# Performance work log

Measured on AMD Instinct MI355X. Metric: run time of the kernel, lower is better.

Reference implementation:

```python
import jax, jax.numpy as jnp
import numpy as np

NUM_HEADS = 12

def setup_inputs() -> dict:
    key = jax.random.key(0)
    k1, k2, k3, k4 = jax.random.split(key, 4)
    B, N, C = 8, 4096, 768
    x1 = jax.random.normal(k1, (B, N, C), dtype=jnp.float32)
    x2 = jax.random.normal(k2, (B, N, C), dtype=jnp.float32)
    segfeature = jax.random.normal(k3, (B, N, C), dtype=jnp.float32)
    # nn.Linear(dim, 2*dim, bias=False) weight, stored transposed for y = x @ W
    W_kv = jax.random.normal(k4, (C, 2 * C), dtype=jnp.float32) * (C ** -0.5)
    return {"x1": x1, "x2": x2, "segfeature": segfeature, "W_kv": W_kv}


def reference(x1, x2, segfeature, W_kv):
    B, N, C = x1.shape
    H = NUM_HEADS
    d = C // H
    scale = d ** -0.5
    # queries: [B, H, N, d]
    q1 = x1.reshape(B, N, H, d).transpose(0, 2, 1, 3)
    q2 = x2.reshape(B, N, H, d).transpose(0, 2, 1, 3)
    # kv projection: [B, M, 2C] -> [2, B, H, M, d]
    M = segfeature.shape[1]
    kv = (segfeature @ W_kv).reshape(B, M, 2, H, d).transpose(2, 0, 3, 1, 4)
    k3, v3 = kv[0], kv[1]
    # context matrix: k^T @ v over sequence -> [B, H, d, d]
    ctx = jnp.einsum('bhmd,bhme->bhde', k3, v3) * scale
    ctx = jax.nn.softmax(ctx, axis=-2)
    # apply context to both queries, back to [B, N, C]
    o1 = jnp.einsum('bhnd,bhde->bnhe', q1, ctx).reshape(B, N, C)
    o2 = jnp.einsum('bhnd,bhde->bnhe', q2, ctx).reshape(B, N, C)
    return (o1, o2)
```

## Files before the change

### kernel.cpp

```cpp
#include <hip/hip_runtime.h>

#define DI __device__ __forceinline__

typedef float        f32x4 __attribute__((ext_vector_type(4)));
typedef _Float16     f16x8 __attribute__((ext_vector_type(8)));
typedef unsigned int u32x4 __attribute__((ext_vector_type(4)));
typedef unsigned int u32x2 __attribute__((ext_vector_type(2)));

DI unsigned short f2h(float f){
    _Float16 h = (_Float16)f;
    return __builtin_bit_cast(unsigned short, h);
}

DI void gl_lds16(const void* g, void* l){
    __builtin_amdgcn_global_load_lds(
        (const __attribute__((address_space(1))) unsigned int*)g,
        (__attribute__((address_space(3))) unsigned int*)l, 16, 0, 0);
}

__global__ __launch_bounds__(256) void k_transpose_f16(
    const float* __restrict__ in, unsigned short* __restrict__ o16,
    int rows, int cols, long ibs, long obs)
{
    __shared__ float t[64][65];
    const int b  = blockIdx.z;
    const int r0 = blockIdx.y * 64, c0 = blockIdx.x * 64;
    const int tid = threadIdx.x;
    const float* ib = in + (long)b * ibs;

    #pragma unroll
    for (int i = 0; i < 4; ++i){
        int r  = (tid >> 4) + i * 16;
        int cq = (tid & 15) * 4;
        f32x4 v = *(const f32x4*)&ib[(long)(r0 + r) * cols + c0 + cq];
        t[r][cq+0] = v[0]; t[r][cq+1] = v[1]; t[r][cq+2] = v[2]; t[r][cq+3] = v[3];
    }
    __syncthreads();

    const int c  = tid >> 2;
    const int ms = (tid & 3) * 16;
    unsigned hv[8];
    #pragma unroll
    for (int k2 = 0; k2 < 8; ++k2){
        unsigned short ha = f2h(t[ms + 2*k2 + 0][c]);
        unsigned short hb = f2h(t[ms + 2*k2 + 1][c]);
        hv[k2] = (unsigned)ha | ((unsigned)hb << 16);
    }
    long o = (long)b * obs + (long)(c0 + c) * rows + r0 + ms;
    u32x4 H0 = {hv[0],hv[1],hv[2],hv[3]}, H1 = {hv[4],hv[5],hv[6],hv[7]};
    *(u32x4*)&o16[o]     = H0;
    *(u32x4*)&o16[o + 8] = H1;
}

DI void stage_lds(const unsigned short* __restrict__ src, long stride,
                  int row0, int k0, unsigned short* tile, int tid)
{
    #pragma unroll
    for (int it = 0; it < 4; ++it){
        int D    = (it * 256 + tid) * 16;
        int row  = D >> 7;
        int colb = (D & 127) ^ ((row & 7) << 4);
        const char* g = (const char*)(src + (long)(row0 + row) * stride + k0) + colb;
        gl_lds16(g, (char*)tile + D);
    }
}

DI f16x8 frag_ld(const unsigned short* tile, int row, int kc16)
{
    int logical = (row << 7) + (kc16 << 4);
    int phys    = logical ^ ((row & 7) << 4);
    return *(const f16x8*)((const char*)tile + phys);
}

DI void ldB3(const unsigned short* __restrict__ g0, long S16, long stride,
             int row0, int k0, int tid, f16x8 r0[4], f16x8 r1[4], f16x8 r2[4])
{
    #pragma unroll
    for (int it = 0; it < 4; ++it){
        int D    = (it * 256 + tid) * 16;
        int row  = D >> 7;
        int colb = D & 127;
        long off = (long)(row0 + row) * stride + k0 + (colb >> 1);
        r0[it] = *(const f16x8*)(g0 + off);
        r1[it] = *(const f16x8*)(g0 + S16 + off);
        r2[it] = *(const f16x8*)(g0 + 2 * S16 + off);
    }
}
DI void wrB3(unsigned short* tile, int tid, f16x8 r0[4], f16x8 r1[4], f16x8 r2[4])
{
    #pragma unroll
    for (int it = 0; it < 4; ++it){
        int D    = (it * 256 + tid) * 16;
        int row  = D >> 7;
        int colb = D & 127;
        f16x8 s;
        #pragma unroll
        for (int t = 0; t < 8; ++t)
            s[t] = (_Float16)((float)r0[it][t] + (float)r1[it][t] + (float)r2[it][t]);
        int phys = (D & ~127) | (colb ^ ((row & 7) << 4));
        *(f16x8*)((char*)tile + phys) = s;
    }
}

DI void mfma_tile(const unsigned short* TA, const unsigned short* TB,
                  int wr, int wc, int lane, f32x4 acc[4][4])
{
    #pragma unroll
    for (int ks = 0; ks < 2; ++ks){
        const int kc = ks * 4 + (lane >> 4);
        f16x8 bf[4];
        #pragma unroll
        for (int cf = 0; cf < 4; ++cf)
            bf[cf] = frag_ld(TB, wc + cf * 16 + (lane & 15), kc);
        #pragma unroll
        for (int rf = 0; rf < 4; ++rf){
            f16x8 af = frag_ld(TA, wr + rf * 16 + (lane & 15), kc);
            #pragma unroll
            for (int cf = 0; cf < 4; ++cf)
                acc[rf][cf] = __builtin_amdgcn_mfma_f32_16x16x32_f16(af, bf[cf], acc[rf][cf], 0, 0, 0);
        }
    }
}

DI void kloop(const unsigned short* a, int rowA0, long sA,
              const unsigned short* b, int rowB0, long sB,
              int kbeg, int kend, f32x4 acc[4][4], unsigned short* lds, int tid)
{
    const int lane = tid & 63;
    const int wave = tid >> 6;
    const int wr = (wave >> 1) * 64, wc = (wave & 1) * 64;

    stage_lds(a, sA, rowA0, kbeg, lds,        tid);
    stage_lds(b, sB, rowB0, kbeg, lds + 8192, tid);
    __syncthreads();

    int cur = 0;
    for (int k0 = kbeg; k0 < kend; k0 += 64){
        const unsigned short* TA = lds + cur * 16384;
        const int kn = k0 + 64;
        if (kn < kend){
            unsigned short* NA = lds + (cur ^ 1) * 16384;
            stage_lds(a, sA, rowA0, kn, NA,        tid);
            stage_lds(b, sB, rowB0, kn, NA + 8192, tid);
        }
        mfma_tile(TA, TA + 8192, wr, wc, lane, acc);
        __syncthreads();
        cur ^= 1;
    }
}

__global__ __launch_bounds__(256) void k_gram(
    const unsigned short* __restrict__ X, unsigned short* __restrict__ Gp16)
{
    __shared__ unsigned short lds[4 * 8192];
    const int id  = blockIdx.x;
    const int b   = id & 7;
    const int r   = id >> 3;
    const int ksl = r / 21;
    int q = r % 21;
    int ti = 0, tj = 0;
    #pragma unroll
    for (int i = 0; i < 6; ++i){ int c = 6 - i; if (q < c){ ti = i; tj = i + q; q = -1; break; } q -= c; }

    static const int kb[4] = {0, 1408, 2752, 4096};

    const unsigned short* XB = X + (long)b * 768 * 4096;

    f32x4 acc[4][4];
    #pragma unroll
    for (int i = 0; i < 4; ++i)
        #pragma unroll
        for (int j = 0; j < 4; ++j) acc[i][j] = (f32x4){0.f, 0.f, 0.f, 0.f};

    kloop(XB, ti * 128, 4096, XB, tj * 128, 4096,
          kb[ksl], kb[ksl + 1], acc, lds, threadIdx.x);

    unsigned short* G = Gp16 + ((long)ksl * 8 + b) * 768 * 768;
    const int lane = threadIdx.x & 63, wave = threadIdx.x >> 6;
    const int wr = (wave >> 1) * 64, wc = (wave & 1) * 64;
    #pragma unroll
    for (int rf = 0; rf < 4; ++rf)
        #pragma unroll
        for (int cf = 0; cf < 4; ++cf){
            int gi = ti * 128 + wr + rf * 16 + 4 * (lane >> 4);
            int gj = tj * 128 + wc + cf * 16 + (lane & 15);
            unsigned short h4[4];
            #pragma unroll
            for (int r2 = 0; r2 < 4; ++r2){
                h4[r2] = f2h(acc[rf][cf][r2]);
                G[(long)(gi + r2) * 768 + gj] = h4[r2];
            }
            if (ti != tj){
                u32x2 p = { (unsigned)h4[0] | ((unsigned)h4[1] << 16),
                            (unsigned)h4[2] | ((unsigned)h4[3] << 16) };
                *(u32x2*)(G + (long)gj * 768 + gi) = p;
            }
        }
}

__global__ __launch_bounds__(256) void k_tt(
    const unsigned short* __restrict__ WT, const unsigned short* __restrict__ Gp16,
    unsigned short* __restrict__ TT)
{
    __shared__ unsigned short lds[4 * 8192];
    const long S16 = 4718592;
    const int id = blockIdx.x;
    const int b  = id & 7;
    const int t  = id >> 3;
    const int ti = t % 6, tj = t / 6;
    const int tid = threadIdx.x;

    const unsigned short* A  = WT + (long)768 * 768;
    const unsigned short* G0 = Gp16 + (long)b * 768 * 768;

    f32x4 acc[4][4];
    #pragma unroll
    for (int i = 0; i < 4; ++i)
        #pragma unroll
        for (int j = 0; j < 4; ++j) acc[i][j] = (f32x4){0.f, 0.f, 0.f, 0.f};

    const int lane = tid & 63;
    const int wave = tid >> 6;
    const int wr = (wave >> 1) * 64, wc = (wave & 1) * 64;

    {
        f16x8 r0[4], r1[4], r2[4];
        ldB3(G0, S16, 768, tj * 128, 0, tid, r0, r1, r2);
        stage_lds(A, 768, ti * 128, 0, lds, tid);
        wrB3(lds + 8192, tid, r0, r1, r2);
        __syncthreads();
    }

    int cur = 0;
    for (int k0 = 0; k0 < 768; k0 += 64){
        const unsigned short* TA = lds + cur * 16384;
        const int kn = k0 + 64;
        f16x8 r0[4], r1[4], r2[4];
        if (kn < 768){
            ldB3(G0, S16, 768, tj * 128, kn, tid, r0, r1, r2);
            stage_lds(A, 768, ti * 128, kn, lds + (cur ^ 1) * 16384, tid);
        }
        mfma_tile(TA, TA + 8192, wr, wc, lane, acc);
        if (kn < 768)
            wrB3(lds + (cur ^ 1) * 16384 + 8192, tid, r0, r1, r2);
        __syncthreads();
        cur ^= 1;
    }

    unsigned short* tt = TT + (long)b * 768 * 768;
    #pragma unroll
    for (int rf = 0; rf < 4; ++rf)
        #pragma unroll
        for (int cf = 0; cf < 4; ++cf){
            int gi = ti * 128 + wr + rf * 16 + 4 * (lane >> 4);
            int gj = tj * 128 + wc + cf * 16 + (lane & 15);
            #pragma unroll
            for (int r = 0; r < 4; ++r)
                tt[(long)(gi + r) * 768 + gj] = f2h(acc[rf][cf][r]);
        }
}

__global__ __launch_bounds__(256) void k_ctx(
    const unsigned short* __restrict__ WT, const unsigned short* __restrict__ TT,
    unsigned short* __restrict__ wT)
{
    __shared__ float red[3][64][65];
    const int bh = blockIdx.x;
    const int b = bh / 12, h = bh % 12;
    const int lane = threadIdx.x & 63;
    const int wave = threadIdx.x >> 6;

    const unsigned short* A = WT + (long)(h * 64) * 768;
    const unsigned short* B = TT + (long)b * 768 * 768 + (long)(h * 64) * 768;

    f32x4 acc[4][4];
    #pragma unroll
    for (int i = 0; i < 4; ++i)
        #pragma unroll
        for (int j = 0; j < 4; ++j) acc[i][j] = (f32x4){0.f, 0.f, 0.f, 0.f};

    for (int kc = wave * 6; kc < wave * 6 + 6; ++kc){
        const int k0 = kc * 32 + (lane >> 4) * 8;
        f16x8 af[4], bf[4];
        #pragma unroll
        for (int f = 0; f < 4; ++f){
            long ro = (long)(f * 16 + (lane & 15)) * 768 + k0;
            af[f] = *(const f16x8*)(A + ro);
            bf[f] = *(const f16x8*)(B + ro);
        }
        #pragma unroll
        for (int rf = 0; rf < 4; ++rf)
            #pragma unroll
            for (int cf = 0; cf < 4; ++cf)
                acc[rf][cf] = __builtin_amdgcn_mfma_f32_16x16x32_f16(af[rf], bf[cf], acc[rf][cf], 0, 0, 0);
    }

    if (wave > 0){
        #pragma unroll
        for (int rf = 0; rf < 4; ++rf)
            #pragma unroll
            for (int cf = 0; cf < 4; ++cf)
                #pragma unroll
                for (int r = 0; r < 4; ++r)
                    red[wave - 1][lane][(rf * 4 + cf) * 4 + r] = acc[rf][cf][r];
    }
    __syncthreads();
    if (wave != 0) return;

    #pragma unroll
    for (int rf = 0; rf < 4; ++rf)
        #pragma unroll
        for (int cf = 0; cf < 4; ++cf)
            #pragma unroll
            for (int r = 0; r < 4; ++r){
                int idx = (rf * 4 + cf) * 4 + r;
                acc[rf][cf][r] += red[0][lane][idx] + red[1][lane][idx] + red[2][lane][idx];
            }

    unsigned short* wout = wT + (long)bh * 4096;
    #pragma unroll
    for (int cf = 0; cf < 4; ++cf){
        float pv[16];
        float m = -3.4e38f;
        #pragma unroll
        for (int rf = 0; rf < 4; ++rf)
            #pragma unroll
            for (int r = 0; r < 4; ++r){
                float s = acc[rf][cf][r] * 0.125f;
                pv[rf * 4 + r] = s;
                m = fmaxf(m, s);
            }
        m = fmaxf(m, __shfl_xor(m, 16));
        m = fmaxf(m, __shfl_xor(m, 32));
        float sum = 0.f;
        #pragma unroll
        for (int k = 0; k < 16; ++k){ pv[k] = __expf(pv[k] - m); sum += pv[k]; }
        sum += __shfl_xor(sum, 16);
        sum += __shfl_xor(sum, 32);
        float inv = 1.f / sum;
        int e = cf * 16 + (lane & 15);
        #pragma unroll
        for (int rf = 0; rf < 4; ++rf)
            #pragma unroll
            for (int r = 0; r < 4; ++r){
                int d = rf * 16 + 4 * (lane >> 4) + r;
                wout[e * 64 + d] = f2h(pv[rf * 4 + r] * inv);
            }
    }
}

__global__ __launch_bounds__(256) void k_apply(
    const float* __restrict__ x1, const float* __restrict__ x2,
    const unsigned short* __restrict__ wT, float* __restrict__ out)
{
    __shared__ float ep[4][64][64];
    const int b = blockIdx.z;
    const int h = blockIdx.y >> 1;
    const int src = blockIdx.y & 1;
    const int lane = threadIdx.x & 63, wave = threadIdx.x >> 6;
    const int n0 = blockIdx.x * 256 + wave * 64;

    const float* x = (src ? x2 : x1) + (long)b * 4096 * 768;
    float* o = out + (long)src * 8 * 4096 * 768 + (long)b * 4096 * 768;

    const unsigned short* W = wT + (long)(b * 12 + h) * 4096;
    f16x8 bw[4][2];
    #pragma unroll
    for (int fe = 0; fe < 4; ++fe)
        #pragma unroll
        for (int ks = 0; ks < 2; ++ks)
            bw[fe][ks] = *(const f16x8*)(W + (fe * 16 + (lane & 15)) * 64 + ks * 32 + (lane >> 4) * 8);

    f32x4 acc[4][4];
    #pragma unroll
    for (int i = 0; i < 4; ++i)
        #pragma unroll
        for (int j = 0; j < 4; ++j) acc[i][j] = (f32x4){0.f, 0.f, 0.f, 0.f};

    #pragma unroll
    for (int rf = 0; rf < 4; ++rf){
        const int row = n0 + rf * 16 + (lane & 15);
        const float* xr = x + (long)row * 768 + h * 64 + (lane >> 4) * 8;
        f32x4 v0 = *(const f32x4*)(xr);
        f32x4 v1 = *(const f32x4*)(xr + 4);
        f32x4 v2 = *(const f32x4*)(xr + 32);
        f32x4 v3 = *(const f32x4*)(xr + 36);
        f16x8 a0, a1;
        #pragma unroll
        for (int t = 0; t < 4; ++t){
            a0[t]     = (_Float16)v0[t];
            a0[t + 4] = (_Float16)v1[t];
            a1[t]     = (_Float16)v2[t];
            a1[t + 4] = (_Float16)v3[t];
        }
        #pragma unroll
        for (int fe = 0; fe < 4; ++fe){
            acc[rf][fe] = __builtin_amdgcn_mfma_f32_16x16x32_f16(a0, bw[fe][0], acc[rf][fe], 0, 0, 0);
            acc[rf][fe] = __builtin_amdgcn_mfma_f32_16x16x32_f16(a1, bw[fe][1], acc[rf][fe], 0, 0, 0);
        }
    }

    #pragma unroll
    for (int rf = 0; rf < 4; ++rf)
        #pragma unroll
        for (int fe = 0; fe < 4; ++fe)
            #pragma unroll
            for (int r = 0; r < 4; ++r)
                ep[wave][rf * 16 + 4 * (lane >> 4) + r][fe * 16 + (lane & 15)] = acc[rf][fe][r];

    #pragma unroll
    for (int pass = 0; pass < 16; ++pass){
        int rr = pass * 4 + (lane >> 4);
        f32x4 v = *(const f32x4*)&ep[wave][rr][(lane & 15) * 4];
        *(f32x4*)&o[(long)(n0 + rr) * 768 + h * 64 + (lane & 15) * 4] = v;
    }
}

__global__ void k_sentinel(float* o){ o[0] = 1.0e9f; }

extern "C" void kernel_launch(void* const* d_in, const int* in_sizes, int n_in,
                              void* d_out, int out_size, void* d_ws, size_t ws_size,
                              hipStream_t stream)
{
    (void)in_sizes; (void)n_in; (void)out_size;
    const float* x1  = (const float*)d_in[0];
    const float* x2  = (const float*)d_in[1];
    const float* seg = (const float*)d_in[2];
    const float* Wkv = (const float*)d_in[3];

    char* Wb = (char*)d_ws;
    unsigned short* X    = (unsigned short*)(Wb);
    unsigned short* WT   = (unsigned short*)(Wb + 50331648);
    unsigned short* TT   = (unsigned short*)(Wb + 52690944);
    unsigned short* wT   = (unsigned short*)(Wb + 62128128);
    unsigned short* Gp16 = (unsigned short*)(Wb + 62914560);
    const size_t need = 91226112;

    if (ws_size < need){
        k_sentinel<<<1, 1, 0, stream>>>((float*)d_out);
        return;
    }

    k_transpose_f16<<<dim3(12, 64, 8), 256, 0, stream>>>(
        seg, X, 4096, 768, (long)4096 * 768, (long)768 * 4096);
    k_transpose_f16<<<dim3(24, 12, 1), 256, 0, stream>>>(
        Wkv, WT, 768, 1536, 0, 0);

    k_gram<<<dim3(504), 256, 0, stream>>>(X, Gp16);

    k_tt<<<dim3(288), 256, 0, stream>>>(WT, Gp16, TT);

    k_ctx<<<dim3(96), 256, 0, stream>>>(WT, TT, wT);

    k_apply<<<dim3(16, 24, 8), 256, 0, stream>>>(x1, x2, wT, (float*)d_out);
}
```

Measured before the change: 179.1 us.

## Merge transpose launches, skip duplicate diagonal Gram loads, use nontemporal output stores

The two fp16 transpose launches (segfeature and W_kv) become one kernel whose flat grid picks which tensor each block handles, removing one launch. In the Gram kernel, diagonal tiles (ti==tj) now stage only one operand tile and reuse it for both sides of the MFMA, halving their global-to-LDS traffic. The apply kernel's final output stores become nontemporal so the large output stream does not pollute cache. These are separate small changes, with little added risk beyond the extra branching in the merged prep kernel.

Measured after the change: 173.1 us (median of 2 runs). -3.4%, faster.

```diff
diff --git a/kernel.cpp b/kernel.cpp
--- a/kernel.cpp
+++ b/kernel.cpp
@@ -18,15 +18,25 @@
         (__attribute__((address_space(3))) unsigned int*)l, 16, 0, 0);
 }
 
-__global__ __launch_bounds__(256) void k_transpose_f16(
-    const float* __restrict__ in, unsigned short* __restrict__ o16,
-    int rows, int cols, long ibs, long obs)
+__global__ __launch_bounds__(256) void k_prep(
+    const float* __restrict__ seg, const float* __restrict__ Wkv,
+    unsigned short* __restrict__ X, unsigned short* __restrict__ WT)
 {
     __shared__ float t[64][65];
-    const int b  = blockIdx.z;
-    const int r0 = blockIdx.y * 64, c0 = blockIdx.x * 64;
+    const int gid = blockIdx.x;
+    const float* in; unsigned short* out;
+    int rows, cols, bx, by, bz; long ibs, obs;
+    if (gid < 6144){
+        bz = gid / 768; int r = gid % 768; by = r / 12; bx = r % 12;
+        in = seg; out = X; rows = 4096; cols = 768;
+        ibs = (long)4096 * 768; obs = (long)768 * 4096;
+    } else {
+        int g2 = gid - 6144; by = g2 / 24; bx = g2 % 24; bz = 0;
+        in = Wkv; out = WT; rows = 768; cols = 1536; ibs = 0; obs = 0;
+    }
+    const int r0 = by * 64, c0 = bx * 64;
     const int tid = threadIdx.x;
-    const float* ib = in + (long)b * ibs;
+    const float* ib = in + (long)bz * ibs;
 
     #pragma unroll
     for (int i = 0; i < 4; ++i){
@@ -46,10 +56,10 @@
         unsigned short hb = f2h(t[ms + 2*k2 + 1][c]);
         hv[k2] = (unsigned)ha | ((unsigned)hb << 16);
     }
-    long o = (long)b * obs + (long)(c0 + c) * rows + r0 + ms;
+    long o = (long)bz * obs + (long)(c0 + c) * rows + r0 + ms;
     u32x4 H0 = {hv[0],hv[1],hv[2],hv[3]}, H1 = {hv[4],hv[5],hv[6],hv[7]};
-    *(u32x4*)&o16[o]     = H0;
-    *(u32x4*)&o16[o + 8] = H1;
+    *(u32x4*)&out[o]     = H0;
+    *(u32x4*)&out[o + 8] = H1;
 }
 
 DI void stage_lds(const unsigned short* __restrict__ src, long stride,
@@ -72,36 +82,6 @@
     return *(const f16x8*)((const char*)tile + phys);
 }
 
-DI void ldB3(const unsigned short* __restrict__ g0, long S16, long stride,
-             int row0, int k0, int tid, f16x8 r0[4], f16x8 r1[4], f16x8 r2[4])
-{
-    #pragma unroll
-    for (int it = 0; it < 4; ++it){
-        int D    = (it * 256 + tid) * 16;
-        int row  = D >> 7;
-        int colb = D & 127;
-        long off = (long)(row0 + row) * stride + k0 + (colb >> 1);
-        r0[it] = *(const f16x8*)(g0 + off);
-        r1[it] = *(const f16x8*)(g0 + S16 + off);
-        r2[it] = *(const f16x8*)(g0 + 2 * S16 + off);
-    }
-}
-DI void wrB3(unsigned short* tile, int tid, f16x8 r0[4], f16x8 r1[4], f16x8 r2[4])
-{
-    #pragma unroll
-    for (int it = 0; it < 4; ++it){
-        int D    = (it * 256 + tid) * 16;
-        int row  = D >> 7;
-        int colb = D & 127;
-        f16x8 s;
-        #pragma unroll
-        for (int t = 0; t < 8; ++t)
-            s[t] = (_Float16)((float)r0[it][t] + (float)r1[it][t] + (float)r2[it][t]);
-        int phys = (D & ~127) | (colb ^ ((row & 7) << 4));
-        *(f16x8*)((char*)tile + phys) = s;
-    }
-}
-
 DI void mfma_tile(const unsigned short* TA, const unsigned short* TB,
                   int wr, int wc, int lane, f32x4 acc[4][4])
 {
@@ -119,33 +99,6 @@
             for (int cf = 0; cf < 4; ++cf)
                 acc[rf][cf] = __builtin_amdgcn_mfma_f32_16x16x32_f16(af, bf[cf], acc[rf][cf], 0, 0, 0);
         }
-    }
-}
-
-DI void kloop(const unsigned short* a, int rowA0, long sA,
-              const unsigned short* b, int rowB0, long sB,
-              int kbeg, int kend, f32x4 acc[4][4], unsigned short* lds, int tid)
-{
-    const int lane = tid & 63;
-    const int wave = tid >> 6;
-    const int wr = (wave >> 1) * 64, wc = (wave & 1) * 64;
-
-    stage_lds(a, sA, rowA0, kbeg, lds,        tid);
-    stage_lds(b, sB, rowB0, kbeg, lds + 8192, tid);
-    __syncthreads();
-
-    int cur = 0;
-    for (int k0 = kbeg; k0 < kend; k0 += 64){
-        const unsigned short* TA = lds + cur * 16384;
-        const int kn = k0 + 64;
-        if (kn < kend){
-            unsigned short* NA = lds + (cur ^ 1) * 16384;
-            stage_lds(a, sA, rowA0, kn, NA,        tid);
-            stage_lds(b, sB, rowB0, kn, NA + 8192, tid);
-        }
-        mfma_tile(TA, TA + 8192, wr, wc, lane, acc);
-        __syncthreads();
-        cur ^= 1;
     }
 }
 
@@ -163,8 +116,13 @@
     for (int i = 0; i < 6; ++i){ int c = 6 - i; if (q < c){ ti = i; tj = i + q; q = -1; break; } q -= c; }
 
     static const int kb[4] = {0, 1408, 2752, 4096};
+    const int kbeg = kb[ksl], kend = kb[ksl + 1];
 
     const unsigned short* XB = X + (long)b * 768 * 4096;
+    const int tid  = threadIdx.x;
+    const int lane = tid & 63, wave = tid >> 6;
+    const int wr = (wave >> 1) * 64, wc = (wave & 1) * 64;
+    const bool diag = (ti == tj);
 
     f32x4 acc[4][4];
     #pragma unroll
@@ -172,12 +130,26 @@
         #pragma unroll
         for (int j = 0; j < 4; ++j) acc[i][j] = (f32x4){0.f, 0.f, 0.f, 0.f};
 
-    kloop(XB, ti * 128, 4096, XB, tj * 128, 4096,
-          kb[ksl], kb[ksl + 1], acc, lds, threadIdx.x);
+    stage_lds(XB, 4096, ti * 128, kbeg, lds, tid);
+    if (!diag) stage_lds(XB, 4096, tj * 128, kbeg, lds + 8192, tid);
+    __syncthreads();
+
+    int cur = 0;
+    for (int k0 = kbeg; k0 < kend; k0 += 64){
+        const unsigned short* TA = lds + cur * 16384;
+        const unsigned short* TB = diag ? TA : TA + 8192;
+        const int kn = k0 + 64;
+        if (kn < kend){
+            unsigned short* NA = lds + (cur ^ 1) * 16384;
+            stage_lds(XB, 4096, ti * 128, kn, NA, tid);
+            if (!diag) stage_lds(XB, 4096, tj * 128, kn, NA + 8192, tid);
+        }
+        mfma_tile(TA, TB, wr, wc, lane, acc);
+        __syncthreads();
+        cur ^= 1;
+    }
 
     unsigned short* G = Gp16 + ((long)ksl * 8 + b) * 768 * 768;
-    const int lane = threadIdx.x & 63, wave = threadIdx.x >> 6;
-    const int wr = (wave >> 1) * 64, wc = (wave & 1) * 64;
     #pragma unroll
     for (int rf = 0; rf < 4; ++rf)
         #pragma unroll
@@ -198,6 +170,36 @@
         }
 }
 
+DI void ldB3(const unsigned short* __restrict__ g0, long S16, long stride,
+             int row0, int k0, int tid, f16x8 r0[4], f16x8 r1[4], f16x8 r2[4])
+{
+    #pragma unroll
+    for (int it = 0; it < 4; ++it){
+        int D    = (it * 256 + tid) * 16;
+        int row  = D >> 7;
+        int colb = D & 127;
+        long off = (long)(row0 + row) * stride + k0 + (colb >> 1);
+        r0[it] = *(const f16x8*)(g0 + off);
+        r1[it] = *(const f16x8*)(g0 + S16 + off);
+        r2[it] = *(const f16x8*)(g0 + 2 * S16 + off);
+    }
+}
+DI void wrB3(unsigned short* tile, int tid, f16x8 r0[4], f16x8 r1[4], f16x8 r2[4])
+{
+    #pragma unroll
+    for (int it = 0; it < 4; ++it){
+        int D    = (it * 256 + tid) * 16;
+        int row  = D >> 7;
+        int colb = D & 127;
+        f16x8 s;
+        #pragma unroll
+        for (int t = 0; t < 8; ++t)
+            s[t] = (_Float16)((float)r0[it][t] + (float)r1[it][t] + (float)r2[it][t]);
+        int phys = (D & ~127) | (colb ^ ((row & 7) << 4));
+        *(f16x8*)((char*)tile + phys) = s;
+    }
+}
+
 __global__ __launch_bounds__(256) void k_tt(
     const unsigned short* __restrict__ WT, const unsigned short* __restrict__ Gp16,
     unsigned short* __restrict__ TT)
@@ -412,7 +414,7 @@
     for (int pass = 0; pass < 16; ++pass){
         int rr = pass * 4 + (lane >> 4);
         f32x4 v = *(const f32x4*)&ep[wave][rr][(lane & 15) * 4];
-        *(f32x4*)&o[(long)(n0 + rr) * 768 + h * 64 + (lane & 15) * 4] = v;
+        __builtin_nontemporal_store(v, (f32x4*)&o[(long)(n0 + rr) * 768 + h * 64 + (lane & 15) * 4]);
     }
 }
 
@@ -441,10 +443,7 @@
         return;
     }
 
-    k_transpose_f16<<<dim3(12, 64, 8), 256, 0, stream>>>(
-        seg, X, 4096, 768, (long)4096 * 768, (long)768 * 4096);
-    k_transpose_f16<<<dim3(24, 12, 1), 256, 0, stream>>>(
-        Wkv, WT, 768, 1536, 0, 0);
+    k_prep<<<dim3(6432), 256, 0, stream>>>(seg, Wkv, X, WT);
 
     k_gram<<<dim3(504), 256, 0, stream>>>(X, Gp16);
 
```
